# Optimization experiments

Measured on AMD Instinct MI355X. Metric: run time of the kernel, lower is better.

Reference implementation:

```python
import jax, jax.numpy as jnp
import numpy as np

TEMP = 0.5  # init kwarg `tmp`
NUM_CLASSES = 100


def setup_inputs() -> dict:
    key = jax.random.key(0)
    k1, k2 = jax.random.split(key)
    embedding = jax.random.normal(k1, (8192, 256), dtype=jnp.float32)
    label = jax.random.randint(k2, (8192,), 0, NUM_CLASSES, dtype=jnp.int64)
    return {"embedding": embedding, "label": label}


def reference(embedding, label):
    # Row-normalize -> pairwise cosine similarity [N, N]
    normed = embedding / jnp.linalg.norm(embedding, axis=1, keepdims=True)
    sim = (normed @ normed.T) / TEMP  # already divided by temperature

    N = embedding.shape[0]
    eye = jnp.eye(N, dtype=bool)

    # Denominator: sum of exp(sim) over off-diagonal entries per row
    exp_sim = jnp.exp(sim)
    row_sum = jnp.sum(jnp.where(eye, 0.0, exp_sim), axis=1)  # [N]

    # log(exp(sim_ij) / row_sum_i) = sim_ij - log(row_sum_i)
    log_prob = sim - jnp.log(row_sum)[:, None]

    # Positive mask: same label, i != j
    pos_mask = (label[:, None] == label[None, :]) & ~eye
    n_i = jnp.sum(pos_mask, axis=1)  # positives per anchor

    inner = jnp.sum(jnp.where(pos_mask, log_prob, 0.0), axis=1)  # [N]
    per_anchor = jnp.where(n_i > 0, -inner / jnp.maximum(n_i, 1).astype(sim.dtype), 0.0)
    return jnp.sum(per_anchor)
```

## Files before the change

### kernel.cpp

```cpp
#include <hip/hip_runtime.h>
#include <hip/hip_bf16.h>
#include <stdint.h>

#define N    8192
#define D    256
#define NCLS 100

static constexpr float TEMP    = 0.5f;
static constexpr float SCALE_F = 1.69864360f;
static constexpr float E2      = 7.38905609893065f;
static constexpr float LN2     = 0.69314718055994531f;

typedef float f32x4 __attribute__((ext_vector_type(4)));

__device__ __forceinline__ unsigned short f2bf(float f) {
  union { float f; unsigned int u; } x; x.f = f;
  unsigned int r = x.u + 0x7fffu + ((x.u >> 16) & 1u);
  return (unsigned short)(r >> 16);
}
__device__ __forceinline__ float bf2f(unsigned short b) {
  union { unsigned int u; float f; } x; x.u = ((unsigned int)b) << 16;
  return x.f;
}
__device__ __forceinline__ void gld16(const void* g, void* l) {
  __builtin_amdgcn_global_load_lds(
      (const __attribute__((address_space(1))) unsigned int*)g,
      (__attribute__((address_space(3))) unsigned int*)l, 16, 0, 0);
}

__global__ __launch_bounds__(256) void normalize_kernel(
    const float* __restrict__ emb, const long long* __restrict__ label,
    unsigned short* __restrict__ abf, unsigned char* __restrict__ a8,
    int* __restrict__ cnt, int* __restrict__ list) {
  const int row  = blockIdx.x * 4 + (threadIdx.x >> 6);
  const int lane = threadIdx.x & 63;
  const float4 v = ((const float4*)(emb + (size_t)row * D))[lane];
  float ss = v.x * v.x + v.y * v.y + v.z * v.z + v.w * v.w;
#pragma unroll
  for (int off = 1; off < 64; off <<= 1) ss += __shfl_xor(ss, off);
  const float s = rsqrtf(ss) * SCALE_F;
  const float x = v.x * s, y = v.y * s, z = v.z * s, wv = v.w * s;

  ushort4 o;
  o.x = f2bf(x); o.y = f2bf(y); o.z = f2bf(z); o.w = f2bf(wv);
  ((ushort4*)(abf + (size_t)row * D))[lane] = o;

  int p = __builtin_amdgcn_cvt_pk_fp8_f32(x, y, 0, false);
  p = __builtin_amdgcn_cvt_pk_fp8_f32(z, wv, p, true);
  ((int*)(a8 + (size_t)row * D))[lane] = p;

  if (lane == 0) {
    const int c = (int)label[row];
    const int slot = atomicAdd(cnt + c, 1);
    list[c * 256 + slot] = row;
  }
}

#define TM 128
#define TN 128
#define BKB 128
#define JT 4

__global__ __launch_bounds__(256) void simexp_rowsum_kernel(
    const unsigned char* __restrict__ A, float* __restrict__ rowsum) {
  __shared__ __align__(16) unsigned char sa[TM * BKB];
  __shared__ __align__(16) unsigned char sb[TN * BKB];
  const int tid  = threadIdx.x;
  const int w    = tid >> 6;
  const int lane = tid & 63;
  const int quad = lane >> 4;
  const int l15  = lane & 15;
  const int row0 = blockIdx.y * TM;
  const int jc0  = blockIdx.x * (TN * JT);
  const int wm   = (w & 1) * 64;
  const int wn   = (w >> 1) * 64;
  const int srow = lane >> 3;
  const int sblk = lane & 7;

  float rowpart[4][4];
#pragma unroll
  for (int mt = 0; mt < 4; ++mt)
#pragma unroll
    for (int e = 0; e < 4; ++e) rowpart[mt][e] = 0.f;

  for (int jt = 0; jt < JT; ++jt) {
    const int jbase = jc0 + jt * TN;
    f32x4 acc[4][4];
#pragma unroll
    for (int mt = 0; mt < 4; ++mt)
#pragma unroll
      for (int nt = 0; nt < 4; ++nt) acc[mt][nt] = (f32x4){0.f, 0.f, 0.f, 0.f};

    for (int kc = 0; kc < D; kc += BKB) {
#pragma unroll
      for (int p = 0; p < 4; ++p) {
        const int seg = p * 4 + w;
        const int r   = seg * 8 + srow;
        const int sc  = kc + ((sblk ^ ((r >> 1) & 7)) << 4);
        gld16(A + (size_t)(row0 + r) * D + sc, sa + seg * 1024);
        gld16(A + (size_t)(jbase + r) * D + sc, sb + seg * 1024);
      }
      __syncthreads();
#pragma unroll
      for (int kk = 0; kk < 4; ++kk) {
        const int b16 = kk * 2 + (quad >> 1);
        const int s8  = (quad & 1) * 8;
        long af[4], bf[4];
#pragma unroll
        for (int mt = 0; mt < 4; ++mt) {
          const int m = wm + mt * 16 + l15;
          af[mt] = *(const long*)(sa + m * BKB +
                                  ((b16 ^ ((m >> 1) & 7)) << 4) + s8);
        }
#pragma unroll
        for (int nt = 0; nt < 4; ++nt) {
          const int n = wn + nt * 16 + l15;
          bf[nt] = *(const long*)(sb + n * BKB +
                                  ((b16 ^ ((n >> 1) & 7)) << 4) + s8);
        }
#pragma unroll
        for (int mt = 0; mt < 4; ++mt)
#pragma unroll
          for (int nt = 0; nt < 4; ++nt)
            acc[mt][nt] = __builtin_amdgcn_mfma_f32_16x16x32_fp8_fp8(
                af[mt], bf[nt], acc[mt][nt], 0, 0, 0);
      }
      __syncthreads();
    }

#pragma unroll
    for (int mt = 0; mt < 4; ++mt)
#pragma unroll
      for (int nt = 0; nt < 4; ++nt)
#pragma unroll
        for (int e = 0; e < 4; ++e)
          rowpart[mt][e] += __builtin_amdgcn_exp2f(acc[mt][nt][e]);
  }

#pragma unroll
  for (int mt = 0; mt < 4; ++mt)
#pragma unroll
    for (int e = 0; e < 4; ++e) {
      float v = rowpart[mt][e];
      v += __shfl_xor(v, 1);
      v += __shfl_xor(v, 2);
      v += __shfl_xor(v, 4);
      v += __shfl_xor(v, 8);
      if (l15 == 0)
        atomicAdd(&rowsum[row0 + wm + mt * 16 + quad * 4 + e], v);
    }
}

__global__ __launch_bounds__(256) void finalize_kernel(
    const unsigned short* __restrict__ abf, const float* __restrict__ rowsum,
    const long long* __restrict__ label, const int* __restrict__ cnt,
    const int* __restrict__ list, float* __restrict__ out) {
  __shared__ float red[4];
  __shared__ int rows_l[256];
  const int tid  = threadIdx.x;
  const int w    = tid >> 6;
  const int lane = tid & 63;

  if (blockIdx.x < NCLS) {
    const int c = blockIdx.x;
    const int m = cnt[c];
    if (m <= 1) return;
    if (tid < m) rows_l[tid] = list[c * 256 + tid];
    __syncthreads();
    float acc = 0.f;
    for (int s = 0; s < m; ++s)
      acc += bf2f(abf[(size_t)rows_l[s] * D + tid]);
    float v = acc * acc;
#pragma unroll
    for (int off = 1; off < 64; off <<= 1) v += __shfl_xor(v, off);
    if (lane == 0) red[w] = v;
    __syncthreads();
    if (tid == 0) {
      const float ssq = red[0] + red[1] + red[2] + red[3];
      const float term = (ssq * LN2 - 2.0f * (float)m) / (float)(m - 1);
      atomicAdd(out, -term);
    }
  } else {
    const int i = (blockIdx.x - NCLS) * 256 + tid;
    const int c = (int)label[i];
    float v = 0.f;
    if (cnt[c] > 1)
      v = __builtin_amdgcn_logf(rowsum[i] - E2) * LN2;
#pragma unroll
    for (int off = 1; off < 64; off <<= 1) v += __shfl_xor(v, off);
    if (lane == 0) red[w] = v;
    __syncthreads();
    if (tid == 0)
      atomicAdd(out, red[0] + red[1] + red[2] + red[3]);
  }
}

extern "C" void kernel_launch(void* const* d_in, const int* in_sizes, int n_in,
                              void* d_out, int out_size, void* d_ws,
                              size_t ws_size, hipStream_t stream) {
  const float* emb = (const float*)d_in[0];
  const long long* label = (const long long*)d_in[1];
  float* out = (float*)d_out;

  char* ws = (char*)d_ws;
  unsigned short* abf = (unsigned short*)ws;
  unsigned char* a8 = (unsigned char*)(ws + (size_t)N * D * 2);
  float* rowsum = (float*)(ws + (size_t)N * D * 3);
  int* cnt = (int*)(rowsum + N);
  int* list = cnt + 128;

  hipMemsetAsync(rowsum, 0, (size_t)N * 4 + 128 * 4, stream);
  hipMemsetAsync(out, 0, sizeof(float), stream);

  normalize_kernel<<<N / 4, 256, 0, stream>>>(emb, label, abf, a8, cnt, list);

  dim3 gridB(N / (TN * JT), N / TM);
  simexp_rowsum_kernel<<<gridB, 256, 0, stream>>>(a8, rowsum);

  finalize_kernel<<<NCLS + N / 256, 256, 0, stream>>>(abf, rowsum, label, cnt,
                                                      list, out);
}
```

Before: 133.4 us.

## Store fp8 embeddings in MFMA-fragment-packed layout for contiguous LDS reads

The normalize kernel now writes the fp8 copy in a 16-row panel layout, where each 16x8-byte fragment for a k-slice is contiguous. The sim kernel loads whole panels straight into LDS and reads operands at linear offsets instead of XOR-swizzled addresses. This removes the swizzle arithmetic and is meant to give conflict-free, coalesced fragment loads. In exchange the fp8 buffer is stored in a custom layout, and the LDS reads rely on the 128-byte lane stride being bank-friendly.

Measured after the change: 132.9 us. No clear change (-0.4%).

```diff
diff --git a/kernel.cpp b/kernel.cpp
--- a/kernel.cpp
+++ b/kernel.cpp
@@ -27,6 +27,7 @@
       (const __attribute__((address_space(1))) unsigned int*)g,
       (__attribute__((address_space(3))) unsigned int*)l, 16, 0, 0);
 }
+
 
 __global__ __launch_bounds__(256) void normalize_kernel(
     const float* __restrict__ emb, const long long* __restrict__ label,
@@ -47,7 +48,8 @@
 
   int p = __builtin_amdgcn_cvt_pk_fp8_f32(x, y, 0, false);
   p = __builtin_amdgcn_cvt_pk_fp8_f32(z, wv, p, true);
-  ((int*)(a8 + (size_t)row * D))[lane] = p;
+  *(int*)(a8 + (size_t)(row >> 4) * 4096 + (lane >> 1) * 128 +
+          (row & 15) * 8 + (lane & 1) * 4) = p;
 
   if (lane == 0) {
     const int c = (int)label[row];
@@ -58,13 +60,12 @@
 
 #define TM 128
 #define TN 128
-#define BKB 128
 #define JT 4
 
 __global__ __launch_bounds__(256) void simexp_rowsum_kernel(
     const unsigned char* __restrict__ A, float* __restrict__ rowsum) {
-  __shared__ __align__(16) unsigned char sa[TM * BKB];
-  __shared__ __align__(16) unsigned char sb[TN * BKB];
+  __shared__ __align__(16) unsigned char sa[TM * 128];
+  __shared__ __align__(16) unsigned char sb[TN * 128];
   const int tid  = threadIdx.x;
   const int w    = tid >> 6;
   const int lane = tid & 63;
@@ -72,10 +73,11 @@
   const int l15  = lane & 15;
   const int row0 = blockIdx.y * TM;
   const int jc0  = blockIdx.x * (TN * JT);
+  const int pr0  = row0 >> 4;
+  const int pam  = (w & 1) * 4;
+  const int pbn  = (w >> 1) * 4;
   const int wm   = (w & 1) * 64;
   const int wn   = (w >> 1) * 64;
-  const int srow = lane >> 3;
-  const int sblk = lane & 7;
 
   float rowpart[4][4];
 #pragma unroll
@@ -85,39 +87,35 @@
 
   for (int jt = 0; jt < JT; ++jt) {
     const int jbase = jc0 + jt * TN;
+    const int pj0   = jbase >> 4;
     f32x4 acc[4][4];
 #pragma unroll
     for (int mt = 0; mt < 4; ++mt)
 #pragma unroll
       for (int nt = 0; nt < 4; ++nt) acc[mt][nt] = (f32x4){0.f, 0.f, 0.f, 0.f};
 
-    for (int kc = 0; kc < D; kc += BKB) {
+#pragma unroll
+    for (int kc = 0; kc < 2; ++kc) {
 #pragma unroll
       for (int p = 0; p < 4; ++p) {
-        const int seg = p * 4 + w;
-        const int r   = seg * 8 + srow;
-        const int sc  = kc + ((sblk ^ ((r >> 1) & 7)) << 4);
-        gld16(A + (size_t)(row0 + r) * D + sc, sa + seg * 1024);
-        gld16(A + (size_t)(jbase + r) * D + sc, sb + seg * 1024);
+        const int seg  = p * 4 + w;
+        const int pp   = seg >> 1;
+        const int half = (seg & 1) * 1024;
+        const size_t goff = kc * 2048 + half + lane * 16;
+        gld16(A + (size_t)(pr0 + pp) * 4096 + goff, sa + seg * 1024);
+        gld16(A + (size_t)(pj0 + pp) * 4096 + goff, sb + seg * 1024);
       }
       __syncthreads();
 #pragma unroll
       for (int kk = 0; kk < 4; ++kk) {
-        const int b16 = kk * 2 + (quad >> 1);
-        const int s8  = (quad & 1) * 8;
+        const int fo = (kk * 4 + quad) * 128 + l15 * 8;
         long af[4], bf[4];
 #pragma unroll
-        for (int mt = 0; mt < 4; ++mt) {
-          const int m = wm + mt * 16 + l15;
-          af[mt] = *(const long*)(sa + m * BKB +
-                                  ((b16 ^ ((m >> 1) & 7)) << 4) + s8);
-        }
-#pragma unroll
-        for (int nt = 0; nt < 4; ++nt) {
-          const int n = wn + nt * 16 + l15;
-          bf[nt] = *(const long*)(sb + n * BKB +
-                                  ((b16 ^ ((n >> 1) & 7)) << 4) + s8);
-        }
+        for (int mt = 0; mt < 4; ++mt)
+          af[mt] = *(const long*)(sa + (pam + mt) * 2048 + fo);
+#pragma unroll
+        for (int nt = 0; nt < 4; ++nt)
+          bf[nt] = *(const long*)(sb + (pbn + nt) * 2048 + fo);
 #pragma unroll
         for (int mt = 0; mt < 4; ++mt)
 #pragma unroll
@@ -149,6 +147,7 @@
       if (l15 == 0)
         atomicAdd(&rowsum[row0 + wm + mt * 16 + quad * 4 + e], v);
     }
+  (void)wn;
 }
 
 __global__ __launch_bounds__(256) void finalize_kernel(
```
